# Kernel tuning notes

Measured on AMD Instinct MI355X. Metric: run time of the kernel, lower is better.

## Reference

```python
import jax, jax.numpy as jnp
import numpy as np

B, N, E = 32, 1024, 512   # docs, word-nodes per doc, hyperedges per doc
V = 50001                 # n_node + 1 (padding idx 0)
D = 300                   # initialFeatureSize == n_hid
H = 300                   # hiddenSize (output of gat2)
NEG = -9e15


def _leaky(v, alpha):
    return jnp.where(v > 0, v, alpha * v)


def _hypergat_layer(x, adj, w, w2, w3, a, a2, wc, alpha, concat):
    # x: [B,N,Fin], adj: [B,E,N] 0/1 incidence. Eval mode: dropout = identity.
    Fo = w2.shape[1]
    x4 = x @ w2                                   # [B,N,Fo]
    if w is not None:                             # transfer=True branch
        x = x @ w                                 # [B,N,Fo]
    mask = adj > 0                                # [B,E,N]
    # edge attention: score per node, constant word-context query
    s1 = _leaky(wc @ a[:Fo, 0] + x4 @ a[Fo:, 0], alpha)          # [B,N]
    att_edge = jax.nn.softmax(jnp.where(mask, s1[:, None, :], NEG), axis=2)  # [B,E,N]
    edge = att_edge @ x                           # [B,E,Fo] hyperedge features
    edge4 = edge @ w3                             # [B,E,Fo]
    # node attention: score(node n, edge e) = leaky(x4[n]@a2_top + edge4[e]@a2_bot)
    sc = _leaky((x4 @ a2[:Fo, 0])[:, None, :] + (edge4 @ a2[Fo:, 0])[:, :, None], alpha)  # [B,E,N]
    att_node = jax.nn.softmax(jnp.where(mask, sc, NEG).transpose(0, 2, 1), axis=2)        # [B,N,E]
    node = att_node @ edge                        # [B,N,Fo]
    return jax.nn.elu(node) if concat else node


def setup_inputs() -> dict:
    key = jax.random.key(0)
    ks = jax.random.split(key, 16)
    stdv = 1.0 / np.sqrt(H)  # DocumentGraph.reset_parameters uniform_(-stdv, stdv) on all params
    u = lambda k, shape: jax.random.uniform(k, shape, jnp.float32, -stdv, stdv)
    return dict(
        inputs=jax.random.randint(ks[0], (B, N), 0, V),
        HT=(jax.random.uniform(ks[1], (B, E, N)) < 0.10).astype(jnp.int32),
        emb=u(ks[2], (V, D)),
        w2_1=u(ks[3], (D, D)), w3_1=u(ks[4], (D, D)),
        a_1=u(ks[5], (2 * D, 1)), a2_1=u(ks[6], (2 * D, 1)), wc_1=u(ks[7], (D,)),
        w_2=u(ks[8], (D, H)), w2_2=u(ks[9], (D, H)), w3_2=u(ks[10], (H, H)),
        a_2=u(ks[11], (2 * H, 1)), a2_2=u(ks[12], (2 * H, 1)), wc_2=u(ks[13], (H,)),
    )


def reference(inputs, HT, emb, w2_1, w3_1, a_1, a2_1, wc_1,
              w_2, w2_2, w3_2, a_2, a2_2, wc_2):
    x = emb[inputs]                                # [B,N,D] embedding lookup
    # gat1: transfer=False, concat=True, alpha=0.1
    x = _hypergat_layer(x, HT, None, w2_1, w3_1, a_1, a2_1, wc_1, 0.1, True)
    # gat2: transfer=True, bias=False, concat=False, alpha=0.2
    x = _hypergat_layer(x, HT, w_2, w2_2, w3_2, a_2, a2_2, wc_2, 0.2, False)
    return x
```

## Files before the change

### kernel.cpp

```cpp
#include <hip/hip_runtime.h>
#include <hip/hip_bf16.h>

#define CB 32
#define CN 1024
#define CE 512
#define CD 300
#define EP 320
#define UCAP 320

__global__ void k_embed(const int* __restrict__ idx, const float* __restrict__ emb,
                        float* __restrict__ X) {
    int gid = blockIdx.x * blockDim.x + threadIdx.x;
    const int total = CB * CN * 75;
    if (gid >= total) return;
    int r = gid / 75, c = gid % 75;
    int e = idx[r];
    reinterpret_cast<float4*>(X)[(size_t)r * 75 + c] =
        reinterpret_cast<const float4*>(emb)[(size_t)e * 75 + c];
}

__global__ void k_transpose(const int* __restrict__ HT, unsigned char* __restrict__ HTt) {
    __shared__ int tile[32][33];
    int b = blockIdx.z;
    int e0 = blockIdx.x * 32, n0 = blockIdx.y * 32;
    int tx = threadIdx.x, ty = threadIdx.y;
    for (int i = ty; i < 32; i += 8)
        tile[i][tx] = HT[((size_t)b * CE + e0 + i) * CN + n0 + tx];
    __syncthreads();
    for (int i = ty; i < 32; i += 8)
        HTt[((size_t)b * CN + n0 + i) * CE + e0 + tx] = (unsigned char)(tile[tx][i] > 0 ? 1 : 0);
}

__global__ void k_prep(const float* __restrict__ w2_1, const float* __restrict__ w3_1,
                       const float* __restrict__ a_1, const float* __restrict__ a2_1,
                       const float* __restrict__ w2_2, const float* __restrict__ w3_2,
                       const float* __restrict__ a_2, const float* __restrict__ a2_2,
                       float* __restrict__ vecs) {
    int which = blockIdx.x;
    int t = threadIdx.x;
    if (t >= CD) return;
    const float* W; const float* v;
    switch (which) {
        case 0:  W = w2_1; v = a_1 + CD;  break;
        case 1:  W = w2_1; v = a2_1;      break;
        case 2:  W = w3_1; v = a2_1 + CD; break;
        case 3:  W = w2_2; v = a_2 + CD;  break;
        case 4:  W = w2_2; v = a2_2;      break;
        default: W = w3_2; v = a2_2 + CD; break;
    }
    float s = 0.f;
    for (int j = 0; j < CD; ++j) s += W[(size_t)t * CD + j] * v[j];
    vecs[which * CD + t] = s;
}

__global__ __launch_bounds__(256) void k_gemm300(const float* __restrict__ A,
                                                 const float* __restrict__ W,
                                                 float* __restrict__ C, int M,
                                                 int lda, int ldc) {
    __shared__ float As[64][20];
    __shared__ float Ws[16][68];
    int tid = threadIdx.x;
    int n0 = blockIdx.x * 64, m0 = blockIdx.y * 64;
    int tx = tid & 15, ty = tid >> 4;
    int la_r = tid >> 2, la_c = (tid & 3) << 2;
    int lw_r = tid >> 4, lw_c = (tid & 15) << 2;
    float acc[4][4] = {};
    for (int k0 = 0; k0 < CD; k0 += 16) {
        {
            int kc = k0 + la_c;
            const float* Ap = A + (size_t)(m0 + la_r) * lda + kc;
            float4 av;
            if (kc + 3 < CD) av = *reinterpret_cast<const float4*>(Ap);
            else {
                av.x = kc     < CD ? Ap[0] : 0.f;
                av.y = kc + 1 < CD ? Ap[1] : 0.f;
                av.z = kc + 2 < CD ? Ap[2] : 0.f;
                av.w = 0.f;
            }
            *reinterpret_cast<float4*>(&As[la_r][la_c]) = av;
        }
        {
            int kr = k0 + lw_r;
            float4 wv = {0.f, 0.f, 0.f, 0.f};
            if (kr < CD) {
                const float* Wp = W + (size_t)kr * CD + n0 + lw_c;
                if (n0 + lw_c + 3 < CD) wv = *reinterpret_cast<const float4*>(Wp);
                else {
                    if (n0 + lw_c     < CD) wv.x = Wp[0];
                    if (n0 + lw_c + 1 < CD) wv.y = Wp[1];
                    if (n0 + lw_c + 2 < CD) wv.z = Wp[2];
                }
            }
            *reinterpret_cast<float4*>(&Ws[lw_r][lw_c]) = wv;
        }
        __syncthreads();
#pragma unroll
        for (int k = 0; k < 16; ++k) {
            float av[4];
#pragma unroll
            for (int i = 0; i < 4; ++i) av[i] = As[ty * 4 + i][k];
            float4 bv = *reinterpret_cast<const float4*>(&Ws[k][tx * 4]);
            float bb[4] = {bv.x, bv.y, bv.z, bv.w};
#pragma unroll
            for (int i = 0; i < 4; ++i)
#pragma unroll
                for (int j = 0; j < 4; ++j) acc[i][j] += av[i] * bb[j];
        }
        __syncthreads();
    }
    for (int i = 0; i < 4; ++i) {
        int m = m0 + ty * 4 + i;
        int n = n0 + tx * 4;
        float* Cp = C + (size_t)m * ldc + n;
        if (n + 3 < CD) {
            float4 v = {acc[i][0], acc[i][1], acc[i][2], acc[i][3]};
            *reinterpret_cast<float4*>(Cp) = v;
        } else {
            for (int j = 0; j < 4; ++j) if (n + j < CD) Cp[j] = acc[i][j];
        }
    }
}

__global__ void k_score(const float* __restrict__ X, const float* __restrict__ av,
                        const float* __restrict__ pv, const float* __restrict__ wc,
                        const float* __restrict__ a_orig,
                        float alpha, float* __restrict__ s1, float* __restrict__ p, int M) {
    int gw = (blockIdx.x * blockDim.x + threadIdx.x) >> 6;
    int lane = threadIdx.x & 63;
    if (gw >= M) return;
    const float* row = X + (size_t)gw * CD;
    float d1 = 0.f, d2 = 0.f, dc = 0.f;
    for (int d = lane; d < CD; d += 64) {
        float x = row[d];
        d1 += x * av[d];
        d2 += x * pv[d];
        dc += wc[d] * a_orig[d];
    }
    for (int o = 32; o; o >>= 1) {
        d1 += __shfl_down(d1, o);
        d2 += __shfl_down(d2, o);
        dc += __shfl_down(dc, o);
    }
    if (lane == 0) {
        float v = dc + d1;
        s1[gw] = v > 0.f ? v : alpha * v;
        p[gw] = d2;
    }
}

__global__ __launch_bounds__(1024) void k_bmax(const float* __restrict__ s1,
                                               float* __restrict__ e1) {
    __shared__ float red[16];
    int b = blockIdx.x, t = threadIdx.x;
    float v = s1[b * CN + t];
    float m = v;
    for (int o = 32; o; o >>= 1) m = fmaxf(m, __shfl_xor(m, o));
    if ((t & 63) == 0) red[t >> 6] = m;
    __syncthreads();
    if (t == 0) {
        float mm = red[0];
        for (int i = 1; i < 16; ++i) mm = fmaxf(mm, red[i]);
        red[0] = mm;
    }
    __syncthreads();
    e1[b * CN + t] = __expf(v - red[0]);
}

__global__ __launch_bounds__(256) void k_edge_agg(const int* __restrict__ HT,
        const float* __restrict__ e1, const float* __restrict__ Xs,
        float* __restrict__ edge) {
    int gw = (blockIdx.x * blockDim.x + threadIdx.x) >> 6;
    int lane = threadIdx.x & 63;
    int b = gw >> 9;
    const int* hrow = HT + (size_t)gw * CN;
    const float* e1b = e1 + b * CN;
    const float* Xb = Xs + (size_t)b * CN * CD;
    float acc[5] = {};
    float den = 0.f;
    bool tail = lane < (CD - 256);
    int any = 0;
#pragma unroll
    for (int c = 0; c < 16; ++c) {
        int n0 = c << 6;
        int m = hrow[n0 + lane];
        float wv = e1b[n0 + lane];
        unsigned long long bal = __ballot(m != 0);
        any |= (bal != 0ull);
        while (bal) {
            int j = (int)__ffsll(bal) - 1;
            bal &= bal - 1ull;
            float w = __shfl(wv, j);
            const float* row = Xb + (size_t)(n0 + j) * CD;
            den += w;
            acc[0] += w * row[lane];
            acc[1] += w * row[lane + 64];
            acc[2] += w * row[lane + 128];
            acc[3] += w * row[lane + 192];
            if (tail) acc[4] += w * row[lane + 256];
        }
    }
    float inv = any ? 1.f / den : 0.f;
    float* erow = edge + (size_t)gw * EP;
    erow[lane]       = acc[0] * inv;
    erow[lane + 64]  = acc[1] * inv;
    erow[lane + 128] = acc[2] * inv;
    erow[lane + 192] = acc[3] * inv;
    erow[lane + 256] = tail ? acc[4] * inv : 0.f;
}

__global__ void k_q(const float* __restrict__ E, const float* __restrict__ qvec,
                    float* __restrict__ q, int M) {
    int gw = (blockIdx.x * blockDim.x + threadIdx.x) >> 6;
    int lane = threadIdx.x & 63;
    if (gw >= M) return;
    const float* row = E + (size_t)gw * EP;
    float d2 = 0.f;
    for (int d = lane; d < CD; d += 64) d2 += row[d] * qvec[d];
    for (int o = 32; o; o >>= 1) d2 += __shfl_down(d2, o);
    if (lane == 0) q[gw] = d2;
}

#define ACC16(vv, ww) do { \
    acc[0][0] += (ww).x * (vv).x; acc[0][1] += (ww).x * (vv).y; \
    acc[0][2] += (ww).x * (vv).z; acc[0][3] += (ww).x * (vv).w; \
    acc[1][0] += (ww).y * (vv).x; acc[1][1] += (ww).y * (vv).y; \
    acc[1][2] += (ww).y * (vv).z; acc[1][3] += (ww).y * (vv).w; \
    acc[2][0] += (ww).z * (vv).x; acc[2][1] += (ww).z * (vv).y; \
    acc[2][2] += (ww).z * (vv).z; acc[2][3] += (ww).z * (vv).w; \
    acc[3][0] += (ww).w * (vv).x; acc[3][1] += (ww).w * (vv).y; \
    acc[3][2] += (ww).w * (vv).z; acc[3][3] += (ww).w * (vv).w; \
} while (0)

__global__ __launch_bounds__(320, 8) void k_node_attn(const unsigned char* __restrict__ HTt,
        const float* __restrict__ p, const float* __restrict__ q,
        const float* __restrict__ edge, float alpha, int do_elu, float* __restrict__ out) {
    __shared__ float4 wsc[4][UCAP];
    __shared__ __align__(8) unsigned short ul[4][UCAP];
    __shared__ int ucnt_s[4], flag_s[4];
    __shared__ float gpn[16], gmx[16], gsc[16];
    __shared__ int gct[16];
    int blk = blockIdx.x;
    int b = blk >> 6, n0 = (blk & 63) << 4;
    int tid = threadIdx.x, wv = tid >> 6, lane = tid & 63;
    const float* qb = q + b * CE;

    if (wv < 4) {
        float pn[4]; const unsigned char* mr[4];
#pragma unroll
        for (int k = 0; k < 4; ++k) {
            int n = n0 + 4 * wv + k;
            pn[k] = p[b * CN + n];
            mr[k] = HTt + ((size_t)b * CN + n) * CE;
        }
        float sc[4][8];
        int cnt[4] = {0, 0, 0, 0};
        float mx[4] = {-3.4e38f, -3.4e38f, -3.4e38f, -3.4e38f};
        int ubits = 0;
#pragma unroll
        for (int j = 0; j < 8; ++j) {
            int e = lane + (j << 6);
            float qe = qb[e];
            int many = 0;
#pragma unroll
            for (int k = 0; k < 4; ++k) {
                int m = mr[k][e];
                float v = pn[k] + qe;
                v = v > 0.f ? v : alpha * v;
                v = m ? v : -3.0e38f;
                cnt[k] += m; many |= m;
                mx[k] = fmaxf(mx[k], v);
                sc[k][j] = v;
            }
            ubits |= (many ? 1 : 0) << j;
        }
#pragma unroll
        for (int k = 0; k < 4; ++k) {
            for (int o = 32; o; o >>= 1) {
                mx[k] = fmaxf(mx[k], __shfl_xor(mx[k], o));
                cnt[k] += __shfl_xor(cnt[k], o);
            }
        }
        float scale[4];
#pragma unroll
        for (int k = 0; k < 4; ++k) {
            float s = 0.f;
#pragma unroll
            for (int j = 0; j < 8; ++j) { float w8 = __expf(sc[k][j] - mx[k]); sc[k][j] = w8; s += w8; }
            for (int o = 32; o; o >>= 1) s += __shfl_xor(s, o);
            scale[k] = cnt[k] > 0 ? 1.f / s : 1.f;
        }
        int base = 0;
        unsigned long long lmask = (1ull << lane) - 1ull;
#pragma unroll
        for (int j = 0; j < 8; ++j) {
            unsigned long long bal = __ballot((ubits >> j) & 1);
            if ((ubits >> j) & 1) {
                int off = base + (int)__popcll(bal & lmask);
                if (off < UCAP) {
                    ul[wv][off] = (unsigned short)(lane + (j << 6));
                    wsc[wv][off] = make_float4(sc[0][j] * scale[0], sc[1][j] * scale[1],
                                               sc[2][j] * scale[2], sc[3][j] * scale[3]);
                }
            }
            base += (int)__popcll(bal);
        }
        if (lane == 0) {
            ucnt_s[wv] = base < UCAP ? base : UCAP;
            flag_s[wv] = (cnt[0] == 0) | (cnt[1] == 0) | (cnt[2] == 0) | (cnt[3] == 0) |
                         (base > UCAP);
            gpn[wv*4+0]=pn[0]; gmx[wv*4+0]=mx[0]; gsc[wv*4+0]=scale[0]; gct[wv*4+0]=cnt[0];
            gpn[wv*4+1]=pn[1]; gmx[wv*4+1]=mx[1]; gsc[wv*4+1]=scale[1]; gct[wv*4+1]=cnt[1];
            gpn[wv*4+2]=pn[2]; gmx[wv*4+2]=mx[2]; gsc[wv*4+2]=scale[2]; gct[wv*4+2]=cnt[2];
            gpn[wv*4+3]=pn[3]; gmx[wv*4+3]=mx[3]; gsc[wv*4+3]=scale[3]; gct[wv*4+3]=cnt[3];
        }
    }
    __syncthreads();

    int grp = tid / 80;
    int j4 = tid - grp * 80;
    const float4* eb4 = reinterpret_cast<const float4*>(edge + (size_t)b * CE * EP) + j4;
    int cnt = ucnt_s[grp], bad = flag_s[grp];
    float acc[4][4] = {};
    if (!bad) {
        int i = 0;
        for (; i + 4 <= cnt; i += 4) {
            ushort4 uu = *reinterpret_cast<const ushort4*>(&ul[grp][i]);
            float4 w0 = wsc[grp][i],     w1 = wsc[grp][i + 1];
            float4 w2 = wsc[grp][i + 2], w3 = wsc[grp][i + 3];
            float4 v0 = eb4[(size_t)uu.x * 80], v1 = eb4[(size_t)uu.y * 80];
            float4 v2 = eb4[(size_t)uu.z * 80], v3 = eb4[(size_t)uu.w * 80];
            ACC16(v0, w0); ACC16(v1, w1); ACC16(v2, w2); ACC16(v3, w3);
        }
        for (; i < cnt; ++i) {
            int e = ul[grp][i];
            float4 v = eb4[(size_t)e * 80];
            float4 w = wsc[grp][i];
            ACC16(v, w);
        }
    } else {
        float pn0 = gpn[grp*4+0], mx0 = gmx[grp*4+0], sc0 = gsc[grp*4+0]; int ct0 = gct[grp*4+0];
        float pn1 = gpn[grp*4+1], mx1 = gmx[grp*4+1], sc1 = gsc[grp*4+1]; int ct1 = gct[grp*4+1];
        float pn2 = gpn[grp*4+2], mx2 = gmx[grp*4+2], sc2 = gsc[grp*4+2]; int ct2 = gct[grp*4+2];
        float pn3 = gpn[grp*4+3], mx3 = gmx[grp*4+3], sc3 = gsc[grp*4+3]; int ct3 = gct[grp*4+3];
        const unsigned char* hb = HTt + ((size_t)b * CN + n0 + grp * 4) * CE;
        for (int e = 0; e < CE; ++e) {
            float4 v = eb4[(size_t)e * 80];
            float qe = qb[e];
            float vv, w;
            int m;
            m = hb[e];
            vv = pn0 + qe; vv = vv > 0.f ? vv : alpha * vv;
            w = ct0 == 0 ? (1.f / CE) : (m ? __expf(vv - mx0) * sc0 : 0.f);
            acc[0][0] += w * v.x; acc[0][1] += w * v.y; acc[0][2] += w * v.z; acc[0][3] += w * v.w;
            m = hb[CE + e];
            vv = pn1 + qe; vv = vv > 0.f ? vv : alpha * vv;
            w = ct1 == 0 ? (1.f / CE) : (m ? __expf(vv - mx1) * sc1 : 0.f);
            acc[1][0] += w * v.x; acc[1][1] += w * v.y; acc[1][2] += w * v.z; acc[1][3] += w * v.w;
            m = hb[2 * CE + e];
            vv = pn2 + qe; vv = vv > 0.f ? vv : alpha * vv;
            w = ct2 == 0 ? (1.f / CE) : (m ? __expf(vv - mx2) * sc2 : 0.f);
            acc[2][0] += w * v.x; acc[2][1] += w * v.y; acc[2][2] += w * v.z; acc[2][3] += w * v.w;
            m = hb[3 * CE + e];
            vv = pn3 + qe; vv = vv > 0.f ? vv : alpha * vv;
            w = ct3 == 0 ? (1.f / CE) : (m ? __expf(vv - mx3) * sc3 : 0.f);
            acc[3][0] += w * v.x; acc[3][1] += w * v.y; acc[3][2] += w * v.z; acc[3][3] += w * v.w;
        }
    }
    if (j4 < 75) {
#pragma unroll
        for (int ni = 0; ni < 4; ++ni) {
            float4 o = {acc[ni][0], acc[ni][1], acc[ni][2], acc[ni][3]};
            if (do_elu) {
                o.x = o.x > 0.f ? o.x : expm1f(o.x);
                o.y = o.y > 0.f ? o.y : expm1f(o.y);
                o.z = o.z > 0.f ? o.z : expm1f(o.z);
                o.w = o.w > 0.f ? o.w : expm1f(o.w);
            }
            *reinterpret_cast<float4*>(out + ((size_t)b * CN + n0 + grp * 4 + ni) * CD + j4 * 4) = o;
        }
    }
}

extern "C" void kernel_launch(void* const* d_in, const int* in_sizes, int n_in,
                              void* d_out, int out_size, void* d_ws, size_t ws_size,
                              hipStream_t stream) {
    const int*   inputs = (const int*)d_in[0];
    const int*   HT     = (const int*)d_in[1];
    const float* emb    = (const float*)d_in[2];
    const float* w2_1   = (const float*)d_in[3];
    const float* w3_1   = (const float*)d_in[4];
    const float* a_1    = (const float*)d_in[5];
    const float* a2_1   = (const float*)d_in[6];
    const float* wc_1   = (const float*)d_in[7];
    const float* w_2    = (const float*)d_in[8];
    const float* w2_2   = (const float*)d_in[9];
    const float* w3_2   = (const float*)d_in[10];
    const float* a_2    = (const float*)d_in[11];
    const float* a2_2   = (const float*)d_in[12];
    const float* wc_2   = (const float*)d_in[13];

    char* ws = (char*)d_ws;
    float* big0         = (float*)(ws);
    float* big1         = (float*)(ws + 39321600);
    float* edge         = (float*)(ws + 78643200);
    unsigned char* HTt  = (unsigned char*)(ws + 99614720);
    float* s1           = (float*)(ws + 116391936);
    float* p            = (float*)(ws + 116523008);
    float* e1           = (float*)(ws + 116654080);
    float* qv           = (float*)(ws + 116785152);
    float* vecs         = (float*)(ws + 116850688);

    k_embed<<<9600, 256, 0, stream>>>(inputs, emb, big0);
    k_transpose<<<dim3(16, 32, 32), dim3(32, 8), 0, stream>>>(HT, HTt);
    k_prep<<<6, 320, 0, stream>>>(w2_1, w3_1, a_1, a2_1, w2_2, w3_2, a_2, a2_2, vecs);

    k_score<<<CB * CN / 4, 256, 0, stream>>>(big0, vecs, vecs + CD, wc_1, a_1, 0.1f, s1, p, CB * CN);
    k_bmax<<<CB, 1024, 0, stream>>>(s1, e1);
    k_edge_agg<<<4096, 256, 0, stream>>>(HT, e1, big0, edge);
    k_q<<<CB * CE / 4, 256, 0, stream>>>(edge, vecs + 2 * CD, qv, CB * CE);
    k_node_attn<<<2048, 320, 0, stream>>>(HTt, p, qv, edge, 0.1f, 1, big0);

    k_score<<<CB * CN / 4, 256, 0, stream>>>(big0, vecs + 3 * CD, vecs + 4 * CD, wc_2, a_2, 0.2f, s1, p, CB * CN);
    k_gemm300<<<dim3(5, 512), 256, 0, stream>>>(big0, w_2, big1, CB * CN, CD, CD);
    k_bmax<<<CB, 1024, 0, stream>>>(s1, e1);
    k_edge_agg<<<4096, 256, 0, stream>>>(HT, e1, big1, edge);
    k_q<<<CB * CE / 4, 256, 0, stream>>>(edge, vecs + 5 * CD, qv, CB * CE);
    k_node_attn<<<2048, 320, 0, stream>>>(HTt, p, qv, edge, 0.2f, 0, (float*)d_out);
}
```

Before: 673.1 us.

## Pack incidence masks into bitsets, fuse q-dot into edge aggregation, swizzle blocks

Precomputes 64-bit ballot bitmasks of the incidence matrix in both edge-major and node-major orientation. The edge aggregation and node attention kernels then read these compact bitsets instead of int32 and byte masks. The separate k_q kernel is folded into edge aggregation, and block indices are remapped so that concurrently running blocks spread across batches. This cuts mask read traffic in four hot kernels and removes one launch, at the cost of two extra one-time bit-packing kernels.

```diff
diff --git a/kernel.cpp b/kernel.cpp
--- a/kernel.cpp
+++ b/kernel.cpp
@@ -29,6 +29,28 @@
     __syncthreads();
     for (int i = ty; i < 32; i += 8)
         HTt[((size_t)b * CN + n0 + i) * CE + e0 + tx] = (unsigned char)(tile[tx][i] > 0 ? 1 : 0);
+}
+
+__global__ void k_ebits(const int* __restrict__ HT, unsigned long long* __restrict__ ebits) {
+    int gw = (blockIdx.x * blockDim.x + threadIdx.x) >> 6;
+    int lane = threadIdx.x & 63;
+    const int* hrow = HT + (size_t)gw * CN;
+#pragma unroll
+    for (int c = 0; c < 16; ++c) {
+        unsigned long long bal = __ballot(hrow[(c << 6) + lane] != 0);
+        if (lane == 0) ebits[(size_t)gw * 16 + c] = bal;
+    }
+}
+
+__global__ void k_nbits(const unsigned char* __restrict__ HTt, unsigned long long* __restrict__ nbits) {
+    int row = (blockIdx.x * blockDim.x + threadIdx.x) >> 6;
+    int lane = threadIdx.x & 63;
+    const unsigned char* hrow = HTt + (size_t)row * CE;
+#pragma unroll
+    for (int c = 0; c < 8; ++c) {
+        unsigned long long bal = __ballot(hrow[(c << 6) + lane] != 0);
+        if (lane == 0) nbits[(size_t)row * 8 + c] = bal;
+    }
 }
 
 __global__ void k_prep(const float* __restrict__ w2_1, const float* __restrict__ w3_1,
@@ -166,13 +188,16 @@
     e1[b * CN + t] = __expf(v - red[0]);
 }
 
-__global__ __launch_bounds__(256) void k_edge_agg(const int* __restrict__ HT,
+__global__ __launch_bounds__(256) void k_edge_agg(const unsigned long long* __restrict__ ebits,
         const float* __restrict__ e1, const float* __restrict__ Xs,
-        float* __restrict__ edge) {
-    int gw = (blockIdx.x * blockDim.x + threadIdx.x) >> 6;
+        const float* __restrict__ qvec, float* __restrict__ edge, float* __restrict__ q) {
+    int i = blockIdx.x;
+    int r = i & 7, t = i >> 3;
+    int b = (t >> 7) * 8 + r;
+    int j = t & 127;
+    int gw = b * CE + (j << 2) + (threadIdx.x >> 6);
     int lane = threadIdx.x & 63;
-    int b = gw >> 9;
-    const int* hrow = HT + (size_t)gw * CN;
+    const unsigned long long* eb = ebits + (size_t)gw * 16;
     const float* e1b = e1 + b * CN;
     const float* Xb = Xs + (size_t)b * CN * CD;
     float acc[5] = {};
@@ -182,15 +207,14 @@
 #pragma unroll
     for (int c = 0; c < 16; ++c) {
         int n0 = c << 6;
-        int m = hrow[n0 + lane];
         float wv = e1b[n0 + lane];
-        unsigned long long bal = __ballot(m != 0);
+        unsigned long long bal = eb[c];
         any |= (bal != 0ull);
         while (bal) {
-            int j = (int)__ffsll(bal) - 1;
+            int jj = (int)__ffsll(bal) - 1;
             bal &= bal - 1ull;
-            float w = __shfl(wv, j);
-            const float* row = Xb + (size_t)(n0 + j) * CD;
+            float w = __shfl(wv, jj);
+            const float* row = Xb + (size_t)(n0 + jj) * CD;
             den += w;
             acc[0] += w * row[lane];
             acc[1] += w * row[lane + 64];
@@ -201,21 +225,18 @@
     }
     float inv = any ? 1.f / den : 0.f;
     float* erow = edge + (size_t)gw * EP;
-    erow[lane]       = acc[0] * inv;
-    erow[lane + 64]  = acc[1] * inv;
-    erow[lane + 128] = acc[2] * inv;
-    erow[lane + 192] = acc[3] * inv;
-    erow[lane + 256] = tail ? acc[4] * inv : 0.f;
-}
-
-__global__ void k_q(const float* __restrict__ E, const float* __restrict__ qvec,
-                    float* __restrict__ q, int M) {
-    int gw = (blockIdx.x * blockDim.x + threadIdx.x) >> 6;
-    int lane = threadIdx.x & 63;
-    if (gw >= M) return;
-    const float* row = E + (size_t)gw * EP;
-    float d2 = 0.f;
-    for (int d = lane; d < CD; d += 64) d2 += row[d] * qvec[d];
+    float o0 = acc[0] * inv, o1 = acc[1] * inv, o2 = acc[2] * inv, o3 = acc[3] * inv;
+    float o4 = tail ? acc[4] * inv : 0.f;
+    erow[lane]       = o0;
+    erow[lane + 64]  = o1;
+    erow[lane + 128] = o2;
+    erow[lane + 192] = o3;
+    erow[lane + 256] = o4;
+    float d2 = o0 * qvec[lane];
+    d2 += o1 * qvec[lane + 64];
+    d2 += o2 * qvec[lane + 128];
+    d2 += o3 * qvec[lane + 192];
+    if (tail) d2 += o4 * qvec[lane + 256];
     for (int o = 32; o; o >>= 1) d2 += __shfl_down(d2, o);
     if (lane == 0) q[gw] = d2;
 }
@@ -231,7 +252,7 @@
     acc[3][2] += (ww).w * (vv).z; acc[3][3] += (ww).w * (vv).w; \
 } while (0)
 
-__global__ __launch_bounds__(320, 8) void k_node_attn(const unsigned char* __restrict__ HTt,
+__global__ __launch_bounds__(320, 8) void k_node_attn(const unsigned long long* __restrict__ nbits,
         const float* __restrict__ p, const float* __restrict__ q,
         const float* __restrict__ edge, float alpha, int do_elu, float* __restrict__ out) {
     __shared__ float4 wsc[4][UCAP];
@@ -239,18 +260,20 @@
     __shared__ int ucnt_s[4], flag_s[4];
     __shared__ float gpn[16], gmx[16], gsc[16];
     __shared__ int gct[16];
-    int blk = blockIdx.x;
-    int b = blk >> 6, n0 = (blk & 63) << 4;
+    int i0 = blockIdx.x;
+    int rr = i0 & 7, tt = i0 >> 3;
+    int b = (tt >> 6) * 8 + rr;
+    int n0 = (tt & 63) << 4;
     int tid = threadIdx.x, wv = tid >> 6, lane = tid & 63;
     const float* qb = q + b * CE;
 
     if (wv < 4) {
-        float pn[4]; const unsigned char* mr[4];
+        float pn[4]; const unsigned long long* nb[4];
 #pragma unroll
         for (int k = 0; k < 4; ++k) {
             int n = n0 + 4 * wv + k;
             pn[k] = p[b * CN + n];
-            mr[k] = HTt + ((size_t)b * CN + n) * CE;
+            nb[k] = nbits + ((size_t)b * CN + n) * 8;
         }
         float sc[4][8];
         int cnt[4] = {0, 0, 0, 0};
@@ -263,7 +286,7 @@
             int many = 0;
 #pragma unroll
             for (int k = 0; k < 4; ++k) {
-                int m = mr[k][e];
+                int m = (int)((nb[k][j] >> lane) & 1ull);
                 float v = pn[k] + qe;
                 v = v > 0.f ? v : alpha * v;
                 v = m ? v : -3.0e38f;
@@ -338,32 +361,23 @@
             ACC16(v, w);
         }
     } else {
-        float pn0 = gpn[grp*4+0], mx0 = gmx[grp*4+0], sc0 = gsc[grp*4+0]; int ct0 = gct[grp*4+0];
-        float pn1 = gpn[grp*4+1], mx1 = gmx[grp*4+1], sc1 = gsc[grp*4+1]; int ct1 = gct[grp*4+1];
-        float pn2 = gpn[grp*4+2], mx2 = gmx[grp*4+2], sc2 = gsc[grp*4+2]; int ct2 = gct[grp*4+2];
-        float pn3 = gpn[grp*4+3], mx3 = gmx[grp*4+3], sc3 = gsc[grp*4+3]; int ct3 = gct[grp*4+3];
-        const unsigned char* hb = HTt + ((size_t)b * CN + n0 + grp * 4) * CE;
+        float pnk[4], mxk[4], sck[4]; int ctk[4];
+        const unsigned long long* nbr[4];
+#pragma unroll
+        for (int k = 0; k < 4; ++k) {
+            pnk[k] = gpn[grp*4+k]; mxk[k] = gmx[grp*4+k]; sck[k] = gsc[grp*4+k]; ctk[k] = gct[grp*4+k];
+            nbr[k] = nbits + ((size_t)b * CN + n0 + grp * 4 + k) * 8;
+        }
         for (int e = 0; e < CE; ++e) {
             float4 v = eb4[(size_t)e * 80];
             float qe = qb[e];
-            float vv, w;
-            int m;
-            m = hb[e];
-            vv = pn0 + qe; vv = vv > 0.f ? vv : alpha * vv;
-            w = ct0 == 0 ? (1.f / CE) : (m ? __expf(vv - mx0) * sc0 : 0.f);
-            acc[0][0] += w * v.x; acc[0][1] += w * v.y; acc[0][2] += w * v.z; acc[0][3] += w * v.w;
-            m = hb[CE + e];
-            vv = pn1 + qe; vv = vv > 0.f ? vv : alpha * vv;
-            w = ct1 == 0 ? (1.f / CE) : (m ? __expf(vv - mx1) * sc1 : 0.f);
-            acc[1][0] += w * v.x; acc[1][1] += w * v.y; acc[1][2] += w * v.z; acc[1][3] += w * v.w;
-            m = hb[2 * CE + e];
-            vv = pn2 + qe; vv = vv > 0.f ? vv : alpha * vv;
-            w = ct2 == 0 ? (1.f / CE) : (m ? __expf(vv - mx2) * sc2 : 0.f);
-            acc[2][0] += w * v.x; acc[2][1] += w * v.y; acc[2][2] += w * v.z; acc[2][3] += w * v.w;
-            m = hb[3 * CE + e];
-            vv = pn3 + qe; vv = vv > 0.f ? vv : alpha * vv;
-            w = ct3 == 0 ? (1.f / CE) : (m ? __expf(vv - mx3) * sc3 : 0.f);
-            acc[3][0] += w * v.x; acc[3][1] += w * v.y; acc[3][2] += w * v.z; acc[3][3] += w * v.w;
+#pragma unroll
+            for (int k = 0; k < 4; ++k) {
+                int m = (int)((nbr[k][e >> 6] >> (e & 63)) & 1ull);
+                float vv = pnk[k] + qe; vv = vv > 0.f ? vv : alpha * vv;
+                float w = ctk[k] == 0 ? (1.f / CE) : (m ? __expf(vv - mxk[k]) * sck[k] : 0.f);
+                acc[k][0] += w * v.x; acc[k][1] += w * v.y; acc[k][2] += w * v.z; acc[k][3] += w * v.w;
+            }
         }
     }
     if (j4 < 75) {
@@ -400,30 +414,32 @@
     const float* wc_2   = (const float*)d_in[13];
 
     char* ws = (char*)d_ws;
-    float* big0         = (float*)(ws);
-    float* big1         = (float*)(ws + 39321600);
-    float* edge         = (float*)(ws + 78643200);
-    unsigned char* HTt  = (unsigned char*)(ws + 99614720);
-    float* s1           = (float*)(ws + 116391936);
-    float* p            = (float*)(ws + 116523008);
-    float* e1           = (float*)(ws + 116654080);
-    float* qv           = (float*)(ws + 116785152);
-    float* vecs         = (float*)(ws + 116850688);
+    float* big0                   = (float*)(ws);
+    float* big1                   = (float*)(ws + 39321600);
+    float* edge                   = (float*)(ws + 78643200);
+    unsigned char* HTt            = (unsigned char*)(ws + 99614720);
+    unsigned long long* ebits     = (unsigned long long*)(ws + 116391936);
+    unsigned long long* nbits     = (unsigned long long*)(ws + 118489088);
+    float* s1                     = (float*)(ws + 120586240);
+    float* p                      = (float*)(ws + 120717312);
+    float* e1                     = (float*)(ws + 120848384);
+    float* qv                     = (float*)(ws + 120979456);
+    float* vecs                   = (float*)(ws + 121044992);
 
     k_embed<<<9600, 256, 0, stream>>>(inputs, emb, big0);
     k_transpose<<<dim3(16, 32, 32), dim3(32, 8), 0, stream>>>(HT, HTt);
+    k_ebits<<<4096, 256, 0, stream>>>(HT, ebits);
+    k_nbits<<<8192, 256, 0, stream>>>(HTt, nbits);
     k_prep<<<6, 320, 0, stream>>>(w2_1, w3_1, a_1, a2_1, w2_2, w3_2, a_2, a2_2, vecs);
 
     k_score<<<CB * CN / 4, 256, 0, stream>>>(big0, vecs, vecs + CD, wc_1, a_1, 0.1f, s1, p, CB * CN);
     k_bmax<<<CB, 1024, 0, stream>>>(s1, e1);
-    k_edge_agg<<<4096, 256, 0, stream>>>(HT, e1, big0, edge);
-    k_q<<<CB * CE / 4, 256, 0, stream>>>(edge, vecs + 2 * CD, qv, CB * CE);
-    k_node_attn<<<2048, 320, 0, stream>>>(HTt, p, qv, edge, 0.1f, 1, big0);
+    k_edge_agg<<<4096, 256, 0, stream>>>(ebits, e1, big0, vecs + 2 * CD, edge, qv);
+    k_node_attn<<<2048, 320, 0, stream>>>(nbits, p, qv, edge, 0.1f, 1, big0);
 
     k_score<<<CB * CN / 4, 256, 0, stream>>>(big0, vecs + 3 * CD, vecs + 4 * CD, wc_2, a_2, 0.2f, s1, p, CB * CN);
     k_gemm300<<<dim3(5, 512), 256, 0, stream>>>(big0, w_2, big1, CB * CN, CD, CD);
     k_bmax<<<CB, 1024, 0, stream>>>(s1, e1);
-    k_edge_agg<<<4096, 256, 0, stream>>>(HT, e1, big1, edge);
-    k_q<<<CB * CE / 4, 256, 0, stream>>>(edge, vecs + 5 * CD, qv, CB * CE);
-    k_node_attn<<<2048, 320, 0, stream>>>(HTt, p, qv, edge, 0.2f, 0, (float*)d_out);
-}
+    k_edge_agg<<<4096, 256, 0, stream>>>(ebits, e1, big1, vecs + 5 * CD, edge, qv);
+    k_node_attn<<<2048, 320, 0, stream>>>(nbits, p, qv, edge, 0.2f, 0, (float*)d_out);
+}
```

Measured after the change: 675.1 us. No clear change (+0.3%).
